# Performance work log

Hardware: AMD Instinct MI355X
Metric: run time of the kernel (lower is better)

The kernel has to match this reference:

```python
import jax, jax.numpy as jnp
import numpy as np

B, D, C, H = 2048, 32, 128, 512  # batch, n_dimension, context_dim, hidden
IN = D + 1 + C  # theta + time + context = 161


def setup_inputs() -> dict:
    key = jax.random.key(0)
    ks = jax.random.split(key, 6)
    theta0 = jax.random.normal(ks[0], (B, D), jnp.float32)  # base N(0,1) sample
    context = jax.random.normal(ks[1], (B, C), jnp.float32)
    W1 = jax.random.normal(ks[2], (IN, 2 * H), jnp.float32) / np.sqrt(IN)
    b1 = jnp.zeros((2 * H,), jnp.float32)
    W2 = jax.random.normal(ks[3], (H, 2 * H), jnp.float32) / np.sqrt(H)
    b2 = jnp.zeros((2 * H,), jnp.float32)
    W3 = jax.random.normal(ks[4], (H, D), jnp.float32) / np.sqrt(H)
    b3 = jnp.zeros((D,), jnp.float32)
    return dict(theta0=theta0, context=context, W1=W1, b1=b1, W2=W2, b2=b2,
                W3=W3, b3=b3, n_steps=16)


def reference(theta0, context, W1, b1, W2, b2, W3, b3, n_steps):
    dt = jnp.float32(1.0 / n_steps)

    def vf(theta, t):
        # network(theta, time, context): GLU-MLP vector field
        tcol = jnp.full((theta.shape[0], 1), t, theta.dtype)
        x = jnp.concatenate([theta, tcol, context], axis=-1)  # [B, D+1+C]
        h = jax.nn.glu(x @ W1 + b1, axis=-1)  # [B, H]
        h = jax.nn.glu(h @ W2 + b2, axis=-1)  # [B, H]
        return h @ W3 + b3  # [B, D]

    def step(theta, i):
        t = i * dt
        k1 = vf(theta, t)
        k2 = vf(theta + 0.5 * dt * k1, t + 0.5 * dt)
        k3 = vf(theta + 0.5 * dt * k2, t + 0.5 * dt)
        k4 = vf(theta + dt * k3, t + dt)
        theta = theta + (dt / 6.0) * (k1 + 2.0 * k2 + 2.0 * k3 + k4)
        return theta, None

    theta, _ = jax.lax.scan(step, theta0, jnp.arange(n_steps, dtype=jnp.float32))
    return theta
```

## Files before the change

### kernel.cpp

```cpp
#include <hip/hip_runtime.h>
#include <hip/hip_bf16.h>

#define THREADS 512
#define NBLK 256
#define NGRP 32
#define GROWS 64
#define IMGU (173*512)
#define H1OFF  (8*IMGU*2)
#define H1SZ   (NGRP*64*1024)
#define KPOFF  (H1OFF + H1SZ)
#define KPSZ   (NGRP*8*4096)
#define CNTOFF (KPOFF + KPSZ)

typedef float f32x4 __attribute__((ext_vector_type(4)));
typedef int   i32x2 __attribute__((ext_vector_type(2)));
typedef __bf16 bf16x8 __attribute__((ext_vector_type(8)));
typedef unsigned short u16x4 __attribute__((ext_vector_type(4)));

static __device__ __forceinline__ unsigned short f2bfu(float f) {
    __hip_bfloat16 h = __float2bfloat16(f);
    unsigned short u; __builtin_memcpy(&u, &h, 2); return u;
}
static __device__ __forceinline__ float bfu2f(unsigned short u) {
    unsigned int x = ((unsigned int)u) << 16;
    float f; __builtin_memcpy(&f, &x, 4); return f;
}

#define MFMA(a, b, c) __builtin_amdgcn_mfma_f32_16x16x32_bf16((a), (b), (c), 0, 0, 0)
#define BC(x)  __builtin_bit_cast(bf16x8, (x))
#define BC2(x) __builtin_bit_cast(i32x2, (x))
#define BCU(x) __builtin_bit_cast(u16x4, (x))

#define LOADG(dst, addr) \
    asm volatile("global_load_dwordx4 %0, %1, off sc1" : "=v"(dst) : "v"(addr))
#define LOADC2(dst, addr) \
    asm volatile("global_load_dwordx2 %0, %1, off sc1" : "=v"(dst) : "v"(addr))
#define STOREC8(addr, val) \
    asm volatile("global_store_dwordx2 %0, %1, off sc1" :: "v"(addr), "v"(val) : "memory")
#define SBAR() __builtin_amdgcn_sched_barrier(0)

__global__ void zero_cnt(unsigned* c) { c[blockIdx.x * 256 + threadIdx.x] = 0u; }

__global__ void pack_members(const float* __restrict__ W1, const float* __restrict__ W2,
                             const float* __restrict__ W3, const float* __restrict__ b1,
                             const float* __restrict__ b2, const float* __restrict__ b3,
                             unsigned short* __restrict__ dst) {
    int b = blockIdx.x, m = b / 173, fi = b % 173, lane = threadIdx.x;
    unsigned short* base = dst + (size_t)m * IMGU;
    if (fi == 172) {
        unsigned short* vb = base + 172 * 512;
        for (int i = lane; i < 384; i += 64) {
            int region = i >> 6, o = i & 63;
            int cA = m * 64 + o, cB = 512 + m * 64 + o;
            float v = 0.f;
            if (region == 0) v = W1[32 * 1024 + cA];
            else if (region == 1) v = W1[32 * 1024 + cB];
            else if (region == 2) v = b1[cA];
            else if (region == 3) v = b1[cB];
            else if (region == 4) v = b2[cA];
            else                  v = b2[cB];
            vb[i] = f2bfu(v);
        }
        if (lane < 32) ((float*)(vb + 384))[lane] = b3[lane];
        return;
    }
    const float* W; int kbase, n, N;
    if (fi < 128) {
        int kt = fi >> 3, ntl = fi & 7;
        int ntg = (ntl < 4) ? (m * 4 + ntl) : (32 + m * 4 + (ntl - 4));
        W = W2; N = 1024; kbase = kt * 32; n = ntg * 16 + (lane & 15);
    } else if (fi < 160) {
        int fj = fi - 128, ktc = fj >> 3, ntl = fj & 7;
        int ntg = (ntl < 4) ? (m * 4 + ntl) : (32 + m * 4 + (ntl - 4));
        W = W1 + 33 * 1024; N = 1024; kbase = ktc * 32; n = ntg * 16 + (lane & 15);
    } else if (fi < 168) {
        int ntl = fi - 160;
        int ntg = (ntl < 4) ? (m * 4 + ntl) : (32 + m * 4 + (ntl - 4));
        W = W1; N = 1024; kbase = 0; n = ntg * 16 + (lane & 15);
    } else {
        int fj = fi - 168, ktl = fj >> 1, nt3 = fj & 1;
        W = W3; N = 32; kbase = m * 64 + ktl * 32; n = nt3 * 16 + (lane & 15);
    }
    kbase += (lane >> 4) * 8;
    union { unsigned short s[8]; int4 v; } u;
#pragma unroll
    for (int j = 0; j < 8; j++) u.s[j] = f2bfu(W[(size_t)(kbase + j) * N + n]);
    *reinterpret_cast<int4*>(base + (size_t)fi * 512 + lane * 8) = u.v;
}

static __device__ __forceinline__ void group_sync(unsigned* c, unsigned tgt) {
    __syncthreads();
    if (threadIdx.x == 0) {
        asm volatile("s_waitcnt vmcnt(0)" ::: "memory");
        __hip_atomic_fetch_add(c, 1u, __ATOMIC_RELAXED, __HIP_MEMORY_SCOPE_AGENT);
        int gd = 0;
        while (__hip_atomic_load(c, __ATOMIC_RELAXED, __HIP_MEMORY_SCOPE_AGENT) < tgt) {
            __builtin_amdgcn_s_sleep(2);
            if (++gd > (1 << 22)) break;
        }
    }
    __syncthreads();
}

__global__ __launch_bounds__(THREADS, 2)
void ccnf_main(const float* __restrict__ theta0,
               const float* __restrict__ ctx,
               char* __restrict__ wsb,
               const int* __restrict__ nsteps_p,
               float* __restrict__ out)
{
    __shared__ __align__(16) unsigned short w2s[128 * 512];
    __shared__ __align__(16) unsigned short cxts[32 * 64 * 4];
    __shared__ __align__(16) unsigned short h2s[8 * 512];
    __shared__ __align__(16) unsigned short als[2048];

    const int tid = threadIdx.x;
    const int lane = tid & 63, wv = tid >> 6;
    const int rt = wv & 3, nh = wv >> 2;
    const int r16 = lane & 15, wq = lane >> 4, rb4 = wq * 4;
    const int row = rt * 16 + r16;
    const int g = blockIdx.x & 31, m = blockIdx.x >> 5;
    const int row0 = g * GROWS;

    const unsigned short* img = (const unsigned short*)wsb + (size_t)m * IMGU;
    unsigned short* h1u = (unsigned short*)(wsb + H1OFF) + (size_t)g * (64 * 512);
    unsigned short* kpu = (unsigned short*)(wsb + KPOFF) + (size_t)g * (8 * 2048);
    unsigned* cnt = (unsigned*)(wsb + CNTOFF) + g * 64;
    const char* h1lane = (const char*)h1u + lane * 16;

    bf16x8 w1aA[2], w1aB[2], w3f[2];
    u16x4 w1tA[2], w1tB[2], b1A[2], b1B[2], b2A[2], b2B[2];
#pragma unroll
    for (int k = 0; k < 2; ++k) {
        w1aA[k] = *(const bf16x8*)(img + (160 + 2 * nh + k) * 512 + lane * 8);
        w1aB[k] = *(const bf16x8*)(img + (164 + 2 * nh + k) * 512 + lane * 8);
        w3f[k]  = *(const bf16x8*)(img + (168 + k * 2 + nh) * 512 + lane * 8);
        int cl = (2 * nh + k) * 16 + rb4;
        const unsigned short* vu = img + 172 * 512;
        w1tA[k] = *(const u16x4*)(vu + cl);       w1tB[k] = *(const u16x4*)(vu + 64 + cl);
        b1A[k]  = *(const u16x4*)(vu + 128 + cl); b1B[k]  = *(const u16x4*)(vu + 192 + cl);
        b2A[k]  = *(const u16x4*)(vu + 256 + cl); b2B[k]  = *(const u16x4*)(vu + 320 + cl);
    }
    const int rowc = tid >> 3, db = (tid & 7) * 4;
    const float4 b3v = *(const float4*)((const float*)(img + 172 * 512 + 384) + db);

#pragma unroll
    for (int q = 0; q < 4; ++q) {
        int idx = wv * 4 + q;
        __builtin_amdgcn_global_load_lds(
            (const __attribute__((address_space(1))) void*)((const char*)img + (size_t)(128 + idx) * 1024 + lane * 16),
            (__attribute__((address_space(3))) void*)(w2s + idx * 512), 16, 0, 0);
    }
    {
        const float* cp = ctx + (size_t)(row0 + rowc) * 128 + (tid & 7) * 16;
        float4 v0 = ((const float4*)cp)[0], v1 = ((const float4*)cp)[1];
        float4 v2 = ((const float4*)cp)[2], v3 = ((const float4*)cp)[3];
        int c0 = (tid & 7) * 16;
        unsigned short* sb = w2s + 16384 + (c0 >> 5) * 2048 + ((c0 & 31) >> 3) * 512 + rowc * 8;
        u16x4 o;
        o[0]=f2bfu(v0.x); o[1]=f2bfu(v0.y); o[2]=f2bfu(v0.z); o[3]=f2bfu(v0.w); *(u16x4*)(sb) = o;
        o[0]=f2bfu(v1.x); o[1]=f2bfu(v1.y); o[2]=f2bfu(v1.z); o[3]=f2bfu(v1.w); *(u16x4*)(sb + 4) = o;
        o[0]=f2bfu(v2.x); o[1]=f2bfu(v2.y); o[2]=f2bfu(v2.z); o[3]=f2bfu(v2.w); *(u16x4*)(sb + 512) = o;
        o[0]=f2bfu(v3.x); o[1]=f2bfu(v3.y); o[2]=f2bfu(v3.z); o[3]=f2bfu(v3.w); *(u16x4*)(sb + 516) = o;
    }
    float th[4], acck[4];
    {
        float4 t0 = *(const float4*)(theta0 + (size_t)(row0 + rowc) * 32 + db);
        th[0]=t0.x; th[1]=t0.y; th[2]=t0.z; th[3]=t0.w;
        acck[0]=acck[1]=acck[2]=acck[3]=0.f;
        u16x4 xo; xo[0]=f2bfu(t0.x); xo[1]=f2bfu(t0.y); xo[2]=f2bfu(t0.z); xo[3]=f2bfu(t0.w);
        *(u16x4*)(als + (db >> 3) * 512 + rowc * 8 + (db & 7)) = xo;
    }
    const int nst = nsteps_p[0];
    const float dt = 1.0f / (float)nst;
    __syncthreads();

#pragma unroll
    for (int ab = 0; ab < 2; ++ab)
#pragma unroll
        for (int k = 0; k < 2; ++k) {
            int ntl = ab * 4 + 2 * nh + k;
            f32x4 a = {0.f, 0.f, 0.f, 0.f};
#pragma unroll
            for (int ktc = 0; ktc < 4; ++ktc) {
                bf16x8 cf = *(const bf16x8*)(w2s + 16384 + ktc * 2048 + wq * 512 + row * 8);
                bf16x8 wf = *(const bf16x8*)(w2s + (ktc * 8 + ntl) * 512 + lane * 8);
                a = MFMA(wf, cf, a);
            }
            u16x4 o;
#pragma unroll
            for (int i = 0; i < 4; ++i) o[i] = f2bfu(a[i]);
            int z4 = ab * 16 + (2 * nh + k) * 4 + wq;
            *(u16x4*)(cxts + (z4 * 64 + row) * 4) = o;
        }
    __syncthreads();

#pragma unroll
    for (int q = 0; q < 16; ++q) {
        int idx = wv * 16 + q;
        __builtin_amdgcn_global_load_lds(
            (const __attribute__((address_space(1))) void*)((const char*)img + (size_t)idx * 1024 + lane * 16),
            (__attribute__((address_space(3))) void*)(w2s + idx * 512), 16, 0, 0);
    }
    __syncthreads();

    const int ne = 4 * nst;
    for (int e = 0; e < ne; ++e) {
        const int s = e & 3;
        const float tt = (float)(e >> 2) * dt + ((s == 0) ? 0.f : (s == 3) ? dt : 0.5f * dt);

        {
            bf16x8 xf = *(const bf16x8*)(als + wq * 512 + row * 8);
            unsigned short* fb = h1u + ((2 * m + nh) * 4 + rt) * 512;
#pragma unroll
            for (int k = 0; k < 2; ++k) {
                f32x4 z = {0.f, 0.f, 0.f, 0.f};
                f32x4 zA = MFMA(w1aA[k], xf, z);
                f32x4 zB = MFMA(w1aB[k], xf, z);
                int zA4 = (2 * nh + k) * 4 + wq, zB4 = 16 + zA4;
                u16x4 cA = *(const u16x4*)(cxts + (zA4 * 64 + row) * 4);
                u16x4 cB = *(const u16x4*)(cxts + (zB4 * 64 + row) * 4);
                u16x4 o;
#pragma unroll
                for (int i = 0; i < 4; ++i) {
                    float va = zA[i] + bfu2f(cA[i]) + bfu2f(b1A[k][i]) + tt * bfu2f(w1tA[k][i]);
                    float vb = zB[i] + bfu2f(cB[i]) + bfu2f(b1B[k][i]) + tt * bfu2f(w1tB[k][i]);
                    o[i] = f2bfu(va * (1.f / (1.f + __expf(-vb))));
                }
                STOREC8(fb + (k * 2 + (wq >> 1)) * 128 + r16 * 8 + (wq & 1) * 4, BC2(o));
            }
        }
        group_sync(&cnt[0], 8u * (unsigned)(e + 1));

        {
            f32x4 acc[4];
#pragma unroll
            for (int p = 0; p < 4; ++p) { f32x4 z = {0.f,0.f,0.f,0.f}; acc[p] = z; }
            f32x4 gb[8];
#pragma unroll
            for (int q = 0; q < 8; ++q) LOADG(gb[q], h1lane + (q * 4 + rt) * 1024);
#pragma unroll
            for (int kt = 0; kt < 16; ++kt) {
                if (kt <= 8)       asm volatile("s_waitcnt vmcnt(7)" ::: "memory");
                else if (kt == 9)  asm volatile("s_waitcnt vmcnt(6)" ::: "memory");
                else if (kt == 10) asm volatile("s_waitcnt vmcnt(5)" ::: "memory");
                else if (kt == 11) asm volatile("s_waitcnt vmcnt(4)" ::: "memory");
                else if (kt == 12) asm volatile("s_waitcnt vmcnt(3)" ::: "memory");
                else if (kt == 13) asm volatile("s_waitcnt vmcnt(2)" ::: "memory");
                else if (kt == 14) asm volatile("s_waitcnt vmcnt(1)" ::: "memory");
                else               asm volatile("s_waitcnt vmcnt(0)" ::: "memory");
                SBAR();
                bf16x8 hf = BC(gb[kt & 7]);
                acc[0] = MFMA(*(const bf16x8*)(w2s + (kt * 8 + 2 * nh + 0) * 512 + lane * 8), hf, acc[0]);
                acc[1] = MFMA(*(const bf16x8*)(w2s + (kt * 8 + 2 * nh + 1) * 512 + lane * 8), hf, acc[1]);
                acc[2] = MFMA(*(const bf16x8*)(w2s + (kt * 8 + 4 + 2 * nh + 0) * 512 + lane * 8), hf, acc[2]);
                acc[3] = MFMA(*(const bf16x8*)(w2s + (kt * 8 + 4 + 2 * nh + 1) * 512 + lane * 8), hf, acc[3]);
                SBAR();
                if (kt < 8) LOADG(gb[kt & 7], h1lane + ((kt + 8) * 4 + rt) * 1024);
            }
#pragma unroll
            for (int k = 0; k < 2; ++k) {
                u16x4 o;
#pragma unroll
                for (int i = 0; i < 4; ++i) {
                    float va = acc[k][i] + bfu2f(b2A[k][i]);
                    float vb = acc[2 + k][i] + bfu2f(b2B[k][i]);
                    o[i] = f2bfu(va * (1.f / (1.f + __expf(-vb))));
                }
                *(u16x4*)(h2s + (nh * 4 + rt) * 512 + (k * 2 + (wq >> 1)) * 128 + r16 * 8 + (wq & 1) * 4) = o;
            }
        }
        __syncthreads();

        {
            f32x4 a3 = {0.f, 0.f, 0.f, 0.f};
#pragma unroll
            for (int ktl = 0; ktl < 2; ++ktl) {
                bf16x8 hf = *(const bf16x8*)(h2s + (ktl * 4 + rt) * 512 + lane * 8);
                a3 = MFMA(w3f[ktl], hf, a3);
            }
            u16x4 o;
#pragma unroll
            for (int i = 0; i < 4; ++i) o[i] = f2bfu(a3[i]);
            STOREC8(kpu + m * 2048 + row * 32 + nh * 16 + rb4, BC2(o));
        }
        group_sync(&cnt[1], 8u * (unsigned)(e + 1));

        {
            i32x2 kq[8];
#pragma unroll
            for (int mm = 0; mm < 8; ++mm)
                LOADC2(kq[mm], kpu + mm * 2048 + rowc * 32 + db);
            asm volatile("s_waitcnt vmcnt(0)" ::: "memory");
            SBAR();
            float kv[4] = {b3v.x, b3v.y, b3v.z, b3v.w};
#pragma unroll
            for (int mm = 0; mm < 8; ++mm) {
                u16x4 q = BCU(kq[mm]);
#pragma unroll
                for (int i = 0; i < 4; ++i) kv[i] += bfu2f(q[i]);
            }
            u16x4 xo;
#pragma unroll
            for (int i = 0; i < 4; ++i) {
                float xe;
                if (s == 0)      { acck[i] = kv[i];          xe = th[i] + 0.5f * dt * kv[i]; }
                else if (s == 1) { acck[i] += 2.f * kv[i];   xe = th[i] + 0.5f * dt * kv[i]; }
                else if (s == 2) { acck[i] += 2.f * kv[i];   xe = th[i] + dt * kv[i]; }
                else             { th[i] += (dt / 6.f) * (acck[i] + kv[i]); xe = th[i]; }
                xo[i] = f2bfu(xe);
            }
            *(u16x4*)(als + (db >> 3) * 512 + rowc * 8 + (db & 7)) = xo;
        }
        __syncthreads();
    }

    if (m == 0) {
        float4 o; o.x = th[0]; o.y = th[1]; o.z = th[2]; o.w = th[3];
        *(float4*)(out + (size_t)(row0 + rowc) * 32 + db) = o;
    }
}

extern "C" void kernel_launch(void* const* d_in, const int* in_sizes, int n_in,
                              void* d_out, int out_size, void* d_ws, size_t ws_size,
                              hipStream_t stream) {
    const float* theta0 = (const float*)d_in[0];
    const float* ctx    = (const float*)d_in[1];
    const float* W1     = (const float*)d_in[2];
    const float* b1     = (const float*)d_in[3];
    const float* W2     = (const float*)d_in[4];
    const float* b2     = (const float*)d_in[5];
    const float* W3     = (const float*)d_in[6];
    const float* b3     = (const float*)d_in[7];
    const int*   nst    = (const int*)d_in[8];
    float* out = (float*)d_out;
    char*  ws  = (char*)d_ws;

    zero_cnt<<<8, 256, 0, stream>>>((unsigned*)(ws + CNTOFF));
    pack_members<<<8 * 173, 64, 0, stream>>>(W1, W2, W3, b1, b2, b3, (unsigned short*)ws);
    ccnf_main<<<NBLK, THREADS, 0, stream>>>(theta0, ctx, ws, nst, out);
}
```

Baseline: 380.3 us.

## Replace atomic-counter group barrier with per-block flags and retile layer-2 MFMA

The cross-block group barrier changes from an atomic counter polled by one thread to per-block sequence flags. Each block writes its own flag and all threads poll the eight peer flags with wave-wide votes, which removes atomic contention and the trailing __syncthreads. Separately, the layer-2 GEMM wave tiling changes so each wave covers two row tiles by one column-pair. This halves the LDS weight fragment reads per MFMA, at the cost of twice as many global h1 loads per wave. Ordering now relies on sc1 stores and loads rather than atomics, which could weaken memory visibility guarantees.

Result: slower. 407.3 us (+7.1%).

```diff
diff --git a/kernel.cpp b/kernel.cpp
--- a/kernel.cpp
+++ b/kernel.cpp
@@ -88,18 +88,20 @@
     *reinterpret_cast<int4*>(base + (size_t)fi * 512 + lane * 8) = u.v;
 }
 
-static __device__ __forceinline__ void group_sync(unsigned* c, unsigned tgt) {
+static __device__ __forceinline__ void group_sync(unsigned* flg, int m, unsigned seq) {
     __syncthreads();
-    if (threadIdx.x == 0) {
+    if (threadIdx.x == 0)
+        asm volatile("global_store_dword %0, %1, off sc1" :: "v"(flg + m), "v"(seq) : "memory");
+    const unsigned* fp = flg + (threadIdx.x & 7);
+    unsigned v; int gd = 0;
+    for (;;) {
+        asm volatile("global_load_dword %0, %1, off sc1" : "=v"(v) : "v"(fp));
         asm volatile("s_waitcnt vmcnt(0)" ::: "memory");
-        __hip_atomic_fetch_add(c, 1u, __ATOMIC_RELAXED, __HIP_MEMORY_SCOPE_AGENT);
-        int gd = 0;
-        while (__hip_atomic_load(c, __ATOMIC_RELAXED, __HIP_MEMORY_SCOPE_AGENT) < tgt) {
-            __builtin_amdgcn_s_sleep(2);
-            if (++gd > (1 << 22)) break;
-        }
-    }
-    __syncthreads();
+        if (__all((int)(v >= seq))) break;
+        __builtin_amdgcn_s_sleep(1);
+        if (++gd > (1 << 22)) break;
+    }
+    __builtin_amdgcn_sched_barrier(0);
 }
 
 __global__ __launch_bounds__(THREADS, 2)
@@ -117,6 +119,7 @@
     const int tid = threadIdx.x;
     const int lane = tid & 63, wv = tid >> 6;
     const int rt = wv & 3, nh = wv >> 2;
+    const int np = wv >> 1, rp = wv & 1;
     const int r16 = lane & 15, wq = lane >> 4, rb4 = wq * 4;
     const int row = rt * 16 + r16;
     const int g = blockIdx.x & 31, m = blockIdx.x >> 5;
@@ -125,11 +128,11 @@
     const unsigned short* img = (const unsigned short*)wsb + (size_t)m * IMGU;
     unsigned short* h1u = (unsigned short*)(wsb + H1OFF) + (size_t)g * (64 * 512);
     unsigned short* kpu = (unsigned short*)(wsb + KPOFF) + (size_t)g * (8 * 2048);
-    unsigned* cnt = (unsigned*)(wsb + CNTOFF) + g * 64;
+    unsigned* flg = (unsigned*)(wsb + CNTOFF) + g * 64;
     const char* h1lane = (const char*)h1u + lane * 16;
 
     bf16x8 w1aA[2], w1aB[2], w3f[2];
-    u16x4 w1tA[2], w1tB[2], b1A[2], b1B[2], b2A[2], b2B[2];
+    u16x4 w1tA[2], w1tB[2], b1A[2], b1B[2];
 #pragma unroll
     for (int k = 0; k < 2; ++k) {
         w1aA[k] = *(const bf16x8*)(img + (160 + 2 * nh + k) * 512 + lane * 8);
@@ -139,8 +142,11 @@
         const unsigned short* vu = img + 172 * 512;
         w1tA[k] = *(const u16x4*)(vu + cl);       w1tB[k] = *(const u16x4*)(vu + 64 + cl);
         b1A[k]  = *(const u16x4*)(vu + 128 + cl); b1B[k]  = *(const u16x4*)(vu + 192 + cl);
-        b2A[k]  = *(const u16x4*)(vu + 256 + cl); b2B[k]  = *(const u16x4*)(vu + 320 + cl);
-    }
+    }
+    const unsigned short* vu2 = img + 172 * 512;
+    u16x4 b2An = *(const u16x4*)(vu2 + 256 + np * 16 + rb4);
+    u16x4 b2Bn = *(const u16x4*)(vu2 + 320 + np * 16 + rb4);
+
     const int rowc = tid >> 3, db = (tid & 7) * 4;
     const float4 b3v = *(const float4*)((const float*)(img + 172 * 512 + 384) + db);
 
@@ -230,44 +236,49 @@
                 STOREC8(fb + (k * 2 + (wq >> 1)) * 128 + r16 * 8 + (wq & 1) * 4, BC2(o));
             }
         }
-        group_sync(&cnt[0], 8u * (unsigned)(e + 1));
+        group_sync(flg, m, 2u * (unsigned)e + 1u);
 
         {
-            f32x4 acc[4];
-#pragma unroll
-            for (int p = 0; p < 4; ++p) { f32x4 z = {0.f,0.f,0.f,0.f}; acc[p] = z; }
+            f32x4 accA[2], accB[2];
+            { f32x4 z = {0.f,0.f,0.f,0.f}; accA[0]=z; accA[1]=z; accB[0]=z; accB[1]=z; }
             f32x4 gb[8];
 #pragma unroll
-            for (int q = 0; q < 8; ++q) LOADG(gb[q], h1lane + (q * 4 + rt) * 1024);
+            for (int q = 0; q < 4; ++q) {
+                LOADG(gb[q * 2 + 0], h1lane + (q * 4 + 2 * rp + 0) * 1024);
+                LOADG(gb[q * 2 + 1], h1lane + (q * 4 + 2 * rp + 1) * 1024);
+            }
 #pragma unroll
             for (int kt = 0; kt < 16; ++kt) {
-                if (kt <= 8)       asm volatile("s_waitcnt vmcnt(7)" ::: "memory");
-                else if (kt == 9)  asm volatile("s_waitcnt vmcnt(6)" ::: "memory");
-                else if (kt == 10) asm volatile("s_waitcnt vmcnt(5)" ::: "memory");
-                else if (kt == 11) asm volatile("s_waitcnt vmcnt(4)" ::: "memory");
-                else if (kt == 12) asm volatile("s_waitcnt vmcnt(3)" ::: "memory");
-                else if (kt == 13) asm volatile("s_waitcnt vmcnt(2)" ::: "memory");
-                else if (kt == 14) asm volatile("s_waitcnt vmcnt(1)" ::: "memory");
+                if (kt <= 12)      asm volatile("s_waitcnt vmcnt(6)" ::: "memory");
+                else if (kt == 13) asm volatile("s_waitcnt vmcnt(4)" ::: "memory");
+                else if (kt == 14) asm volatile("s_waitcnt vmcnt(2)" ::: "memory");
                 else               asm volatile("s_waitcnt vmcnt(0)" ::: "memory");
                 SBAR();
-                bf16x8 hf = BC(gb[kt & 7]);
-                acc[0] = MFMA(*(const bf16x8*)(w2s + (kt * 8 + 2 * nh + 0) * 512 + lane * 8), hf, acc[0]);
-                acc[1] = MFMA(*(const bf16x8*)(w2s + (kt * 8 + 2 * nh + 1) * 512 + lane * 8), hf, acc[1]);
-                acc[2] = MFMA(*(const bf16x8*)(w2s + (kt * 8 + 4 + 2 * nh + 0) * 512 + lane * 8), hf, acc[2]);
-                acc[3] = MFMA(*(const bf16x8*)(w2s + (kt * 8 + 4 + 2 * nh + 1) * 512 + lane * 8), hf, acc[3]);
+                bf16x8 wAf = *(const bf16x8*)(w2s + (kt * 8 + np) * 512 + lane * 8);
+                bf16x8 wBf = *(const bf16x8*)(w2s + (kt * 8 + 4 + np) * 512 + lane * 8);
+                bf16x8 hf0 = BC(gb[(kt & 3) * 2 + 0]);
+                bf16x8 hf1 = BC(gb[(kt & 3) * 2 + 1]);
+                accA[0] = MFMA(wAf, hf0, accA[0]);
+                accA[1] = MFMA(wAf, hf1, accA[1]);
+                accB[0] = MFMA(wBf, hf0, accB[0]);
+                accB[1] = MFMA(wBf, hf1, accB[1]);
                 SBAR();
-                if (kt < 8) LOADG(gb[kt & 7], h1lane + ((kt + 8) * 4 + rt) * 1024);
-            }
-#pragma unroll
-            for (int k = 0; k < 2; ++k) {
+                if (kt < 12) {
+                    LOADG(gb[(kt & 3) * 2 + 0], h1lane + ((kt + 4) * 4 + 2 * rp + 0) * 1024);
+                    LOADG(gb[(kt & 3) * 2 + 1], h1lane + ((kt + 4) * 4 + 2 * rp + 1) * 1024);
+                }
+            }
+#pragma unroll
+            for (int u = 0; u < 2; ++u) {
                 u16x4 o;
 #pragma unroll
                 for (int i = 0; i < 4; ++i) {
-                    float va = acc[k][i] + bfu2f(b2A[k][i]);
-                    float vb = acc[2 + k][i] + bfu2f(b2B[k][i]);
+                    float va = accA[u][i] + bfu2f(b2An[i]);
+                    float vb = accB[u][i] + bfu2f(b2Bn[i]);
                     o[i] = f2bfu(va * (1.f / (1.f + __expf(-vb))));
                 }
-                *(u16x4*)(h2s + (nh * 4 + rt) * 512 + (k * 2 + (wq >> 1)) * 128 + r16 * 8 + (wq & 1) * 4) = o;
+                *(u16x4*)(h2s + ((np >> 1) * 4 + 2 * rp + u) * 512
+                          + (((np & 1) * 2 + (wq >> 1)) * 16 + r16) * 8 + (wq & 1) * 4) = o;
             }
         }
         __syncthreads();
@@ -284,7 +295,7 @@
             for (int i = 0; i < 4; ++i) o[i] = f2bfu(a3[i]);
             STOREC8(kpu + m * 2048 + row * 32 + nh * 16 + rb4, BC2(o));
         }
-        group_sync(&cnt[1], 8u * (unsigned)(e + 1));
+        group_sync(flg, m, 2u * (unsigned)e + 2u);
 
         {
             i32x2 kq[8];
```

## Split layer-2 GEMM over K between wave halves with LDS partial-sum reduction

Applied to the files above, without the earlier changes.

Layer 2's work split changes from output-N halves to K halves. Each wave half now loads only its 8 K-tiles of h1 and computes all 8 output tiles, dropping the per-iteration double barriers. The two halves' partial sums are reduced through LDS in bf16, which adds several __syncthreads and a second rounding step. The vmcnt(0) wait before the group-sync atomic is also removed, which risks publishing before the global stores are visible.

New measurement: 414.7 us. +9.1%, slower.

```diff
diff --git a/kernel.cpp b/kernel.cpp
--- a/kernel.cpp
+++ b/kernel.cpp
@@ -91,7 +91,6 @@
 static __device__ __forceinline__ void group_sync(unsigned* c, unsigned tgt) {
     __syncthreads();
     if (threadIdx.x == 0) {
-        asm volatile("s_waitcnt vmcnt(0)" ::: "memory");
         __hip_atomic_fetch_add(c, 1u, __ATOMIC_RELAXED, __HIP_MEMORY_SCOPE_AGENT);
         int gd = 0;
         while (__hip_atomic_load(c, __ATOMIC_RELAXED, __HIP_MEMORY_SCOPE_AGENT) < tgt) {
@@ -129,7 +128,7 @@
     const char* h1lane = (const char*)h1u + lane * 16;
 
     bf16x8 w1aA[2], w1aB[2], w3f[2];
-    u16x4 w1tA[2], w1tB[2], b1A[2], b1B[2], b2A[2], b2B[2];
+    u16x4 w1tA[2], w1tB[2], b1A[2], b1B[2];
 #pragma unroll
     for (int k = 0; k < 2; ++k) {
         w1aA[k] = *(const bf16x8*)(img + (160 + 2 * nh + k) * 512 + lane * 8);
@@ -139,7 +138,13 @@
         const unsigned short* vu = img + 172 * 512;
         w1tA[k] = *(const u16x4*)(vu + cl);       w1tB[k] = *(const u16x4*)(vu + 64 + cl);
         b1A[k]  = *(const u16x4*)(vu + 128 + cl); b1B[k]  = *(const u16x4*)(vu + 192 + cl);
-        b2A[k]  = *(const u16x4*)(vu + 256 + cl); b2B[k]  = *(const u16x4*)(vu + 320 + cl);
+    }
+    u16x4 b2Ar[4], b2Br[4];
+#pragma unroll
+    for (int t = 0; t < 4; ++t) {
+        const unsigned short* vu = img + 172 * 512;
+        b2Ar[t] = *(const u16x4*)(vu + 256 + t * 16 + rb4);
+        b2Br[t] = *(const u16x4*)(vu + 320 + t * 16 + rb4);
     }
     const int rowc = tid >> 3, db = (tid & 7) * 4;
     const float4 b3v = *(const float4*)((const float*)(img + 172 * 512 + 384) + db);
@@ -233,41 +238,80 @@
         group_sync(&cnt[0], 8u * (unsigned)(e + 1));
 
         {
-            f32x4 acc[4];
-#pragma unroll
-            for (int p = 0; p < 4; ++p) { f32x4 z = {0.f,0.f,0.f,0.f}; acc[p] = z; }
+            f32x4 accA[4], accB[4];
+#pragma unroll
+            for (int t = 0; t < 4; ++t) { f32x4 z = {0.f,0.f,0.f,0.f}; accA[t] = z; accB[t] = z; }
             f32x4 gb[8];
 #pragma unroll
-            for (int q = 0; q < 8; ++q) LOADG(gb[q], h1lane + (q * 4 + rt) * 1024);
-#pragma unroll
-            for (int kt = 0; kt < 16; ++kt) {
-                if (kt <= 8)       asm volatile("s_waitcnt vmcnt(7)" ::: "memory");
-                else if (kt == 9)  asm volatile("s_waitcnt vmcnt(6)" ::: "memory");
-                else if (kt == 10) asm volatile("s_waitcnt vmcnt(5)" ::: "memory");
-                else if (kt == 11) asm volatile("s_waitcnt vmcnt(4)" ::: "memory");
-                else if (kt == 12) asm volatile("s_waitcnt vmcnt(3)" ::: "memory");
-                else if (kt == 13) asm volatile("s_waitcnt vmcnt(2)" ::: "memory");
-                else if (kt == 14) asm volatile("s_waitcnt vmcnt(1)" ::: "memory");
-                else               asm volatile("s_waitcnt vmcnt(0)" ::: "memory");
+            for (int q = 0; q < 8; ++q)
+                LOADG(gb[q], h1lane + ((nh * 8 + q) * 4 + rt) * 1024);
+#pragma unroll
+            for (int j = 0; j < 8; ++j) {
+                if (j == 0)      asm volatile("s_waitcnt vmcnt(7)" ::: "memory");
+                else if (j == 1) asm volatile("s_waitcnt vmcnt(6)" ::: "memory");
+                else if (j == 2) asm volatile("s_waitcnt vmcnt(5)" ::: "memory");
+                else if (j == 3) asm volatile("s_waitcnt vmcnt(4)" ::: "memory");
+                else if (j == 4) asm volatile("s_waitcnt vmcnt(3)" ::: "memory");
+                else if (j == 5) asm volatile("s_waitcnt vmcnt(2)" ::: "memory");
+                else if (j == 6) asm volatile("s_waitcnt vmcnt(1)" ::: "memory");
+                else             asm volatile("s_waitcnt vmcnt(0)" ::: "memory");
                 SBAR();
-                bf16x8 hf = BC(gb[kt & 7]);
-                acc[0] = MFMA(*(const bf16x8*)(w2s + (kt * 8 + 2 * nh + 0) * 512 + lane * 8), hf, acc[0]);
-                acc[1] = MFMA(*(const bf16x8*)(w2s + (kt * 8 + 2 * nh + 1) * 512 + lane * 8), hf, acc[1]);
-                acc[2] = MFMA(*(const bf16x8*)(w2s + (kt * 8 + 4 + 2 * nh + 0) * 512 + lane * 8), hf, acc[2]);
-                acc[3] = MFMA(*(const bf16x8*)(w2s + (kt * 8 + 4 + 2 * nh + 1) * 512 + lane * 8), hf, acc[3]);
-                SBAR();
-                if (kt < 8) LOADG(gb[kt & 7], h1lane + ((kt + 8) * 4 + rt) * 1024);
-            }
-#pragma unroll
-            for (int k = 0; k < 2; ++k) {
-                u16x4 o;
-#pragma unroll
-                for (int i = 0; i < 4; ++i) {
-                    float va = acc[k][i] + bfu2f(b2A[k][i]);
-                    float vb = acc[2 + k][i] + bfu2f(b2B[k][i]);
-                    o[i] = f2bfu(va * (1.f / (1.f + __expf(-vb))));
-                }
-                *(u16x4*)(h2s + (nh * 4 + rt) * 512 + (k * 2 + (wq >> 1)) * 128 + r16 * 8 + (wq & 1) * 4) = o;
+                const int kt = nh * 8 + j;
+                bf16x8 hf = BC(gb[j]);
+#pragma unroll
+                for (int t = 0; t < 4; ++t) {
+                    accA[t] = MFMA(*(const bf16x8*)(w2s + (kt * 8 + t) * 512 + lane * 8), hf, accA[t]);
+                    accB[t] = MFMA(*(const bf16x8*)(w2s + (kt * 8 + 4 + t) * 512 + lane * 8), hf, accB[t]);
+                }
+            }
+            if (nh == 1) {
+#pragma unroll
+                for (int t = 0; t < 4; ++t) {
+                    u16x4 o;
+#pragma unroll
+                    for (int i = 0; i < 4; ++i) o[i] = f2bfu(accA[t][i]);
+                    *(u16x4*)(h2s + ((rt * 4 + t) * 64 + lane) * 4) = o;
+                }
+            }
+            __syncthreads();
+            if (nh == 0) {
+#pragma unroll
+                for (int t = 0; t < 4; ++t) {
+                    u16x4 p = *(const u16x4*)(h2s + ((rt * 4 + t) * 64 + lane) * 4);
+#pragma unroll
+                    for (int i = 0; i < 4; ++i) accA[t][i] += bfu2f(p[i]);
+                }
+            }
+            __syncthreads();
+            if (nh == 1) {
+#pragma unroll
+                for (int t = 0; t < 4; ++t) {
+                    u16x4 o;
+#pragma unroll
+                    for (int i = 0; i < 4; ++i) o[i] = f2bfu(accB[t][i]);
+                    *(u16x4*)(h2s + ((rt * 4 + t) * 64 + lane) * 4) = o;
+                }
+            }
+            __syncthreads();
+            u16x4 hres[4];
+            if (nh == 0) {
+#pragma unroll
+                for (int t = 0; t < 4; ++t) {
+                    u16x4 p = *(const u16x4*)(h2s + ((rt * 4 + t) * 64 + lane) * 4);
+#pragma unroll
+                    for (int i = 0; i < 4; ++i) {
+                        float va = accA[t][i] + bfu2f(b2Ar[t][i]);
+                        float vb = accB[t][i] + bfu2f(p[i]) + bfu2f(b2Br[t][i]);
+                        hres[t][i] = f2bfu(va * (1.f / (1.f + __expf(-vb))));
+                    }
+                }
+            }
+            __syncthreads();
+            if (nh == 0) {
+#pragma unroll
+                for (int t = 0; t < 4; ++t)
+                    *(u16x4*)(h2s + ((t >> 1) * 4 + rt) * 512
+                              + (((t & 1) * 2 + (wq >> 1)) * 16 + r16) * 8 + (wq & 1) * 4) = hres[t];
             }
         }
         __syncthreads();
```

## Replace atomic group barrier with per-block flags, double-buffer exchange, stagger loads

Applied to the files above, without the earlier changes.

Swaps the atomic-counter group barrier for per-block flag stores that every wave polls directly with a wave-wide vote. This removes the atomic and the extra __syncthreads round trip. The h1 and k-partial exchange buffers are now double-buffered by step parity so a fast block cannot overwrite data a slow block is still reading. The h1 reads are also rotated per block to spread contention across memory channels. The cost is more polling traffic from all waves and more workspace memory.

Result: no change. 378.0 us (-0.6%).

```diff
diff --git a/kernel.cpp b/kernel.cpp
--- a/kernel.cpp
+++ b/kernel.cpp
@@ -7,10 +7,12 @@
 #define GROWS 64
 #define IMGU (173*512)
 #define H1OFF  (8*IMGU*2)
-#define H1SZ   (NGRP*64*1024)
-#define KPOFF  (H1OFF + H1SZ)
-#define KPSZ   (NGRP*8*4096)
-#define CNTOFF (KPOFF + KPSZ)
+#define H1BUF  65536
+#define H1GRP  (2*H1BUF)
+#define KPOFF  (H1OFF + (size_t)NGRP*H1GRP)
+#define KPBUF  32768
+#define KPGRP  (2*KPBUF)
+#define CNTOFF (KPOFF + (size_t)NGRP*KPGRP)
 
 typedef float f32x4 __attribute__((ext_vector_type(4)));
 typedef int   i32x2 __attribute__((ext_vector_type(2)));
@@ -88,18 +90,17 @@
     *reinterpret_cast<int4*>(base + (size_t)fi * 512 + lane * 8) = u.v;
 }
 
-static __device__ __forceinline__ void group_sync(unsigned* c, unsigned tgt) {
-    __syncthreads();
-    if (threadIdx.x == 0) {
+static __device__ __forceinline__ void wait8(const unsigned* f8, unsigned tgt) {
+    const unsigned* fp = f8 + (threadIdx.x & 7);
+    unsigned v; int gd = 0;
+    for (;;) {
+        asm volatile("global_load_dword %0, %1, off sc1" : "=v"(v) : "v"(fp));
         asm volatile("s_waitcnt vmcnt(0)" ::: "memory");
-        __hip_atomic_fetch_add(c, 1u, __ATOMIC_RELAXED, __HIP_MEMORY_SCOPE_AGENT);
-        int gd = 0;
-        while (__hip_atomic_load(c, __ATOMIC_RELAXED, __HIP_MEMORY_SCOPE_AGENT) < tgt) {
-            __builtin_amdgcn_s_sleep(2);
-            if (++gd > (1 << 22)) break;
-        }
-    }
-    __syncthreads();
+        if (__all((int)(v >= tgt))) break;
+        __builtin_amdgcn_s_sleep(1);
+        if (++gd > (1 << 22)) break;
+    }
+    __builtin_amdgcn_sched_barrier(0);
 }
 
 __global__ __launch_bounds__(THREADS, 2)
@@ -123,10 +124,9 @@
     const int row0 = g * GROWS;
 
     const unsigned short* img = (const unsigned short*)wsb + (size_t)m * IMGU;
-    unsigned short* h1u = (unsigned short*)(wsb + H1OFF) + (size_t)g * (64 * 512);
-    unsigned short* kpu = (unsigned short*)(wsb + KPOFF) + (size_t)g * (8 * 2048);
-    unsigned* cnt = (unsigned*)(wsb + CNTOFF) + g * 64;
-    const char* h1lane = (const char*)h1u + lane * 16;
+    char* h1base = wsb + H1OFF + (size_t)g * H1GRP;
+    char* kpbase = wsb + KPOFF + (size_t)g * KPGRP;
+    unsigned* flg = (unsigned*)(wsb + CNTOFF) + g * 64;
 
     bf16x8 w1aA[2], w1aB[2], w3f[2];
     u16x4 w1tA[2], w1tB[2], b1A[2], b1B[2], b2A[2], b2B[2];
@@ -208,10 +208,14 @@
     for (int e = 0; e < ne; ++e) {
         const int s = e & 3;
         const float tt = (float)(e >> 2) * dt + ((s == 0) ? 0.f : (s == 3) ? dt : 0.5f * dt);
+        const unsigned tgt = (unsigned)(e + 1);
+        unsigned short* h1e = (unsigned short*)(h1base + (e & 1) * H1BUF);
+        unsigned short* kpe = (unsigned short*)(kpbase + (e & 1) * KPBUF);
+        const char* h1lane = (const char*)h1e + lane * 16;
 
         {
             bf16x8 xf = *(const bf16x8*)(als + wq * 512 + row * 8);
-            unsigned short* fb = h1u + ((2 * m + nh) * 4 + rt) * 512;
+            unsigned short* fb = h1e + ((2 * m + nh) * 4 + rt) * 512;
 #pragma unroll
             for (int k = 0; k < 2; ++k) {
                 f32x4 z = {0.f, 0.f, 0.f, 0.f};
@@ -230,7 +234,10 @@
                 STOREC8(fb + (k * 2 + (wq >> 1)) * 128 + r16 * 8 + (wq & 1) * 4, BC2(o));
             }
         }
-        group_sync(&cnt[0], 8u * (unsigned)(e + 1));
+        __syncthreads();
+        if (tid == 0)
+            asm volatile("global_store_dword %0, %1, off sc1" :: "v"(flg + m), "v"(tgt) : "memory");
+        wait8(flg, tgt);
 
         {
             f32x4 acc[4];
@@ -238,25 +245,32 @@
             for (int p = 0; p < 4; ++p) { f32x4 z = {0.f,0.f,0.f,0.f}; acc[p] = z; }
             f32x4 gb[8];
 #pragma unroll
-            for (int q = 0; q < 8; ++q) LOADG(gb[q], h1lane + (q * 4 + rt) * 1024);
-#pragma unroll
-            for (int kt = 0; kt < 16; ++kt) {
-                if (kt <= 8)       asm volatile("s_waitcnt vmcnt(7)" ::: "memory");
-                else if (kt == 9)  asm volatile("s_waitcnt vmcnt(6)" ::: "memory");
-                else if (kt == 10) asm volatile("s_waitcnt vmcnt(5)" ::: "memory");
-                else if (kt == 11) asm volatile("s_waitcnt vmcnt(4)" ::: "memory");
-                else if (kt == 12) asm volatile("s_waitcnt vmcnt(3)" ::: "memory");
-                else if (kt == 13) asm volatile("s_waitcnt vmcnt(2)" ::: "memory");
-                else if (kt == 14) asm volatile("s_waitcnt vmcnt(1)" ::: "memory");
-                else               asm volatile("s_waitcnt vmcnt(0)" ::: "memory");
+            for (int q = 0; q < 8; ++q) {
+                const int qi = (q + 2 * m) & 15;
+                LOADG(gb[q], h1lane + (qi * 4 + rt) * 1024);
+            }
+#pragma unroll
+            for (int j = 0; j < 16; ++j) {
+                if (j <= 8)       asm volatile("s_waitcnt vmcnt(7)" ::: "memory");
+                else if (j == 9)  asm volatile("s_waitcnt vmcnt(6)" ::: "memory");
+                else if (j == 10) asm volatile("s_waitcnt vmcnt(5)" ::: "memory");
+                else if (j == 11) asm volatile("s_waitcnt vmcnt(4)" ::: "memory");
+                else if (j == 12) asm volatile("s_waitcnt vmcnt(3)" ::: "memory");
+                else if (j == 13) asm volatile("s_waitcnt vmcnt(2)" ::: "memory");
+                else if (j == 14) asm volatile("s_waitcnt vmcnt(1)" ::: "memory");
+                else              asm volatile("s_waitcnt vmcnt(0)" ::: "memory");
                 SBAR();
-                bf16x8 hf = BC(gb[kt & 7]);
+                const int kt = (j + 2 * m) & 15;
+                bf16x8 hf = BC(gb[j & 7]);
                 acc[0] = MFMA(*(const bf16x8*)(w2s + (kt * 8 + 2 * nh + 0) * 512 + lane * 8), hf, acc[0]);
                 acc[1] = MFMA(*(const bf16x8*)(w2s + (kt * 8 + 2 * nh + 1) * 512 + lane * 8), hf, acc[1]);
                 acc[2] = MFMA(*(const bf16x8*)(w2s + (kt * 8 + 4 + 2 * nh + 0) * 512 + lane * 8), hf, acc[2]);
                 acc[3] = MFMA(*(const bf16x8*)(w2s + (kt * 8 + 4 + 2 * nh + 1) * 512 + lane * 8), hf, acc[3]);
                 SBAR();
-                if (kt < 8) LOADG(gb[kt & 7], h1lane + ((kt + 8) * 4 + rt) * 1024);
+                if (j < 8) {
+                    const int qi = (j + 8 + 2 * m) & 15;
+                    LOADG(gb[j & 7], h1lane + (qi * 4 + rt) * 1024);
+                }
             }
 #pragma unroll
             for (int k = 0; k < 2; ++k) {
@@ -282,15 +296,18 @@
             u16x4 o;
 #pragma unroll
             for (int i = 0; i < 4; ++i) o[i] = f2bfu(a3[i]);
-            STOREC8(kpu + m * 2048 + row * 32 + nh * 16 + rb4, BC2(o));
-        }
-        group_sync(&cnt[1], 8u * (unsigned)(e + 1));
+            STOREC8(kpe + m * 2048 + row * 32 + nh * 16 + rb4, BC2(o));
+        }
+        __syncthreads();
+        if (tid == 0)
+            asm volatile("global_store_dword %0, %1, off sc1" :: "v"(flg + 8 + m), "v"(tgt) : "memory");
+        wait8(flg + 8, tgt);
 
         {
             i32x2 kq[8];
 #pragma unroll
             for (int mm = 0; mm < 8; ++mm)
-                LOADC2(kq[mm], kpu + mm * 2048 + rowc * 32 + db);
+                LOADC2(kq[mm], kpe + mm * 2048 + rowc * 32 + db);
             asm volatile("s_waitcnt vmcnt(0)" ::: "memory");
             SBAR();
             float kv[4] = {b3v.x, b3v.y, b3v.z, b3v.w};
```
